# Kernel tuning notes

Hardware: AMD Instinct MI355X
Metric: run time of the kernel (lower is better)

## Reference

```python
import jax, jax.numpy as jnp
import numpy as np

IO, LAT, HID, NV = 64, 32, 60, 16

def setup_inputs() -> dict:
    key = jax.random.key(0)
    ks = jax.random.split(key, 11)
    def lin(k, fan_out, fan_in):
        kw, kb = jax.random.split(k)
        bound = 1.0 / np.sqrt(fan_in)
        w = jax.random.uniform(kw, (fan_out, fan_in), jnp.float32, -bound, bound)
        b = jax.random.uniform(kb, (fan_out,), jnp.float32, -bound, bound)
        return w, b
    enc1_w, enc1_b = lin(ks[0], HID, IO)
    mean_w, mean_b = lin(ks[1], LAT, HID)
    std_w, std_b = lin(ks[2], LAT, HID)
    dec1_w, dec1_b = lin(ks[3], HID, LAT)
    dec2_w, dec2_b = lin(ks[4], IO, HID)
    h_input = jax.random.normal(ks[5], (4096, 16, IO), jnp.float32)
    return {"h_input": h_input, "num_traj": 8,
            "enc1_w": enc1_w, "enc1_b": enc1_b, "mean_w": mean_w, "mean_b": mean_b,
            "std_w": std_w, "std_b": std_b, "dec1_w": dec1_w, "dec1_b": dec1_b,
            "dec2_w": dec2_w, "dec2_b": dec2_b}

def reference(h_input, num_traj, enc1_w, enc1_b, mean_w, mean_b, std_w, std_b, dec1_w, dec1_b, dec2_w, dec2_b):
    B, H, _ = h_input.shape
    x = h_input.reshape(-1, IO)               # [N, io]
    N = x.shape[0]
    h1 = jax.nn.relu(x @ enc1_w.T + enc1_b)   # [N, 60]
    mu = h1 @ mean_w.T + mean_b               # [N, L]
    logvar = h1 @ std_w.T + std_b             # [N, L]
    std = jnp.exp(0.5 * logvar)
    eps = jax.random.normal(jax.random.key(1), (num_traj, N, LAT), jnp.float32)
    z = mu[None] + eps * std[None]            # [T, N, L]
    # on-device closed-form standard-normal pdf (replaces scipy host roundtrip)
    log_pdf = -0.5 * (LAT * jnp.log(2.0 * jnp.pi) + jnp.sum(eps * eps, axis=-1))  # [T, N]
    pdf = jnp.exp(log_pdf)
    # decode, batched over trajectories
    h3 = jax.nn.relu(jnp.einsum('tnl,hl->tnh', z, dec1_w) + dec1_b)
    out = jnp.einsum('tnh,oh->tno', h3, dec2_w) + dec2_b          # [T, N, io]
    traj = out.reshape(num_traj, N, H, IO // H).transpose(0, 2, 1, 3)  # [T, H, N, io/H]
    p = jnp.exp(pdf)                          # faithful: exp of the pdf values
    p = p / jnp.sum(p, axis=0)                # normalize over trajectories
    prob_list = p.reshape(num_traj, -1, NV)   # [T, N/NV, NV]
    return traj, mu, logvar, prob_list
```

## Files before the change

kernel.cpp:

```cpp
#include <hip/hip_runtime.h>
#include <cstdint>


#define TPB_A 256
#define NBLK_A 1024
#define TPB_B 256
#define NBLK_B 2048

__device__ __forceinline__ void threefry2x32_01(uint32_t c0, uint32_t c1,
                                                uint32_t& o0, uint32_t& o1) {
  uint32_t x0 = c0;
  uint32_t x1 = c1 + 1u;
#define TFR(r) { x0 += x1; x1 = (x1 << (r)) | (x1 >> (32 - (r))); x1 ^= x0; }
  TFR(13) TFR(15) TFR(26) TFR(6)
  x0 += 1u;          x1 += 0x1BD11BDCu;
  TFR(17) TFR(29) TFR(16) TFR(24)
  x0 += 0x1BD11BDBu; x1 += 2u;
  TFR(13) TFR(15) TFR(26) TFR(6)
        x1 += 4u;
  TFR(17) TFR(29) TFR(16) TFR(24)
  x0 += 1u;          x1 += 0x1BD11BDFu;
  TFR(13) TFR(15) TFR(26) TFR(6)
  x0 += 0x1BD11BDBu; x1 += 5u;
#undef TFR
  o0 = x0; o1 = x1;
}

__device__ __forceinline__ uint32_t threefry_bits_partitionable(uint32_t idx) {
  uint32_t o0, o1;
  threefry2x32_01(0u, idx, o0, o1);
  return o0 ^ o1;
}

__device__ __forceinline__ float bits_to_normal(uint32_t b) {
  const float lo = -0.99999994f;
  float f = __uint_as_float((b >> 9) | 0x3F800000u) - 1.0f;
  float u = fmaxf(f * 2.0f + lo, lo);
  return 1.41421356f * erfinvf(u);
}

__global__ __launch_bounds__(TPB_A, 4) void vae_encode(
    const float* __restrict__ X,
    const float* __restrict__ w1, const float* __restrict__ b1,
    const float* __restrict__ wm, const float* __restrict__ bm,
    const float* __restrict__ wsd, const float* __restrict__ bsd,
    float* __restrict__ out) {
  const int tid = threadIdx.x;
  const int lane = tid & 63;
  const int slot = __builtin_amdgcn_readfirstlane(tid >> 6);
  const int i0 = slot * 8;
  const int n = blockIdx.x * 64 + lane;

  float x[64];
  {
    const float4* xr = (const float4*)(X + (size_t)n * 64);
#pragma unroll
    for (int q = 0; q < 16; ++q) {
      float4 v = xr[q];
      x[4 * q + 0] = v.x; x[4 * q + 1] = v.y;
      x[4 * q + 2] = v.z; x[4 * q + 3] = v.w;
    }
  }

  float mu[8], lv[8];
#pragma unroll
  for (int ii = 0; ii < 8; ++ii) { mu[ii] = bm[i0 + ii]; lv[ii] = bsd[i0 + ii]; }
  for (int j = 0; j < 60; ++j) {
    const float4* wr = (const float4*)(w1 + j * 64);
    float a0 = 0.f, a1 = 0.f, a2 = 0.f, a3 = 0.f;
#pragma unroll
    for (int q = 0; q < 16; ++q) {
      float4 w = wr[q];
      a0 = fmaf(w.x, x[4 * q + 0], a0);
      a1 = fmaf(w.y, x[4 * q + 1], a1);
      a2 = fmaf(w.z, x[4 * q + 2], a2);
      a3 = fmaf(w.w, x[4 * q + 3], a3);
    }
    float h = fmaxf((a0 + a1) + (a2 + a3) + b1[j], 0.f);
    const float* wmc = wm + i0 * 60 + j;
    const float* wsc = wsd + i0 * 60 + j;
#pragma unroll
    for (int ii = 0; ii < 8; ++ii) {
      mu[ii] = fmaf(wmc[ii * 60], h, mu[ii]);
      lv[ii] = fmaf(wsc[ii * 60], h, lv[ii]);
    }
  }

  float4* muo = (float4*)(out + (size_t)33554432 + (size_t)n * 32 + i0);
  float4* lvo = (float4*)(out + (size_t)35651584 + (size_t)n * 32 + i0);
  float4 v0, v1, w0, w1v;
  v0.x = mu[0]; v0.y = mu[1]; v0.z = mu[2]; v0.w = mu[3];
  v1.x = mu[4]; v1.y = mu[5]; v1.z = mu[6]; v1.w = mu[7];
  w0.x = lv[0]; w0.y = lv[1]; w0.z = lv[2]; w0.w = lv[3];
  w1v.x = lv[4]; w1v.y = lv[5]; w1v.z = lv[6]; w1v.w = lv[7];
  muo[0] = v0; muo[1] = v1;
  lvo[0] = w0; lvo[1] = w1v;
}

__global__ __launch_bounds__(TPB_B, 4) void vae_decode(
    const float* __restrict__ wd1, const float* __restrict__ bd1,
    const float* __restrict__ wd2, const float* __restrict__ bd2,
    float* __restrict__ out) {
  const int tid = threadIdx.x;
  const int g = blockIdx.x * TPB_B + tid;
  const int n = g & 65535;
  const int t = g >> 16;

  const float4* mur = (const float4*)(out + (size_t)33554432 + (size_t)n * 32);
  const float4* lvr = (const float4*)(out + (size_t)35651584 + (size_t)n * 32);
  const uint32_t cbase = (uint32_t)t * 2097152u + (uint32_t)n * 32u;
  float z[32];
#pragma unroll
  for (int gq = 0; gq < 8; ++gq) {
    float4 m4 = mur[gq];
    float4 v4 = lvr[gq];
    float s0 = expf(0.5f * v4.x), s1 = expf(0.5f * v4.y);
    float s2 = expf(0.5f * v4.z), s3 = expf(0.5f * v4.w);
    uint32_t c = cbase + (uint32_t)(4 * gq);
    z[4 * gq + 0] = fmaf(bits_to_normal(threefry_bits_partitionable(c + 0u)), s0, m4.x);
    z[4 * gq + 1] = fmaf(bits_to_normal(threefry_bits_partitionable(c + 1u)), s1, m4.y);
    z[4 * gq + 2] = fmaf(bits_to_normal(threefry_bits_partitionable(c + 2u)), s2, m4.z);
    z[4 * gq + 3] = fmaf(bits_to_normal(threefry_bits_partitionable(c + 3u)), s3, m4.w);
  }

  float h3[60];
#pragma unroll
  for (int j = 0; j < 60; ++j) {
    const float* wj = wd1 + j * 32;
    float a = bd1[j];
#pragma unroll
    for (int l = 0; l < 32; ++l) a = fmaf(wj[l], z[l], a);
    h3[j] = fmaxf(a, 0.f);
  }

  {
    float4* trj = (float4*)out + (size_t)(t * 16) * 65536 + n;
    const float4* bd24 = (const float4*)bd2;
    for (int hh = 0; hh < 16; ++hh) {
      const float4* w0 = (const float4*)(wd2 + (hh * 4 + 0) * 60);
      const float4* w1r = (const float4*)(wd2 + (hh * 4 + 1) * 60);
      const float4* w2 = (const float4*)(wd2 + (hh * 4 + 2) * 60);
      const float4* w3 = (const float4*)(wd2 + (hh * 4 + 3) * 60);
      float a0 = 0.f, a1 = 0.f, a2 = 0.f, a3 = 0.f;
#pragma unroll
      for (int q = 0; q < 15; ++q) {
        float4 wa = w0[q], wb = w1r[q], wc = w2[q], wdv = w3[q];
        float h0 = h3[4 * q + 0], hv1 = h3[4 * q + 1];
        float hv2 = h3[4 * q + 2], hv3 = h3[4 * q + 3];
        a0 = fmaf(wa.x, h0, a0); a0 = fmaf(wa.y, hv1, a0);
        a0 = fmaf(wa.z, hv2, a0); a0 = fmaf(wa.w, hv3, a0);
        a1 = fmaf(wb.x, h0, a1); a1 = fmaf(wb.y, hv1, a1);
        a1 = fmaf(wb.z, hv2, a1); a1 = fmaf(wb.w, hv3, a1);
        a2 = fmaf(wc.x, h0, a2); a2 = fmaf(wc.y, hv1, a2);
        a2 = fmaf(wc.z, hv2, a2); a2 = fmaf(wc.w, hv3, a2);
        a3 = fmaf(wdv.x, h0, a3); a3 = fmaf(wdv.y, hv1, a3);
        a3 = fmaf(wdv.z, hv2, a3); a3 = fmaf(wdv.w, hv3, a3);
      }
      float4 bb = bd24[hh];
      float4 o;
      o.x = a0 + bb.x; o.y = a1 + bb.y; o.z = a2 + bb.z; o.w = a3 + bb.w;
      trj[(size_t)hh * 65536] = o;
    }
  }

  out[(size_t)37748736 + (size_t)t * 65536 + (size_t)n] = 0.125f;
}

extern "C" void kernel_launch(void* const* d_in, const int* in_sizes, int n_in,
                              void* d_out, int out_size, void* d_ws, size_t ws_size,
                              hipStream_t stream) {
  const float* X   = (const float*)d_in[0];
  const float* w1  = (const float*)d_in[2];
  const float* b1  = (const float*)d_in[3];
  const float* wm  = (const float*)d_in[4];
  const float* bm  = (const float*)d_in[5];
  const float* wsd = (const float*)d_in[6];
  const float* bsd = (const float*)d_in[7];
  const float* wd1 = (const float*)d_in[8];
  const float* bd1 = (const float*)d_in[9];
  const float* wd2 = (const float*)d_in[10];
  const float* bd2 = (const float*)d_in[11];

  vae_encode<<<NBLK_A, TPB_A, 0, stream>>>(X, w1, b1, wm, bm, wsd, bsd,
                                           (float*)d_out);
  vae_decode<<<NBLK_B, TPB_B, 0, stream>>>(wd1, bd1, wd2, bd2, (float*)d_out);
}
```

Measured before the change: 388.0 us.

## Stage encoder weights in LDS with transposed mean/std layout; limit decoder unrolling

The encoder kernel now copies the first-layer weights and a transposed, interleaved copy of the mean/logvar weights into shared memory. This replaces per-thread global and scalar loads with vectorized LDS reads, cutting the number of weight loads in the inner loop. In the decoder, the hidden-layer loop changes from full unroll to unroll 2 and the output loop gets unroll 2, which may lower register pressure and code size. The costs are a block-level sync and staging work in the encoder, plus possibly less instruction-level parallelism in the decoder.

```diff
diff --git a/kernel.cpp b/kernel.cpp
--- a/kernel.cpp
+++ b/kernel.cpp
@@ -45,12 +45,26 @@
     const float* __restrict__ wm, const float* __restrict__ bm,
     const float* __restrict__ wsd, const float* __restrict__ bsd,
     float* __restrict__ out) {
+  __shared__ alignas(16) float s_w1[3840];
+  __shared__ alignas(16) float s_wmst[3840];
+
   const int tid = threadIdx.x;
   const int lane = tid & 63;
   const int slot = __builtin_amdgcn_readfirstlane(tid >> 6);
   const int i0 = slot * 8;
   const int n = blockIdx.x * 64 + lane;
 
+  {
+    const float4* w14 = (const float4*)w1;
+    float4* s14 = (float4*)s_w1;
+    for (int m = tid; m < 960; m += TPB_A) s14[m] = w14[m];
+    for (int m = tid; m < 3840; m += TPB_A) {
+      int j = m >> 6, i = m & 63;
+      s_wmst[m] = (i < 32) ? wm[i * 60 + j] : wsd[(i - 32) * 60 + j];
+    }
+  }
+  __syncthreads();
+
   float x[64];
   {
     const float4* xr = (const float4*)(X + (size_t)n * 64);
@@ -66,7 +80,7 @@
 #pragma unroll
   for (int ii = 0; ii < 8; ++ii) { mu[ii] = bm[i0 + ii]; lv[ii] = bsd[i0 + ii]; }
   for (int j = 0; j < 60; ++j) {
-    const float4* wr = (const float4*)(w1 + j * 64);
+    const float4* wr = (const float4*)&s_w1[j * 64];
     float a0 = 0.f, a1 = 0.f, a2 = 0.f, a3 = 0.f;
 #pragma unroll
     for (int q = 0; q < 16; ++q) {
@@ -77,13 +91,17 @@
       a3 = fmaf(w.w, x[4 * q + 3], a3);
     }
     float h = fmaxf((a0 + a1) + (a2 + a3) + b1[j], 0.f);
-    const float* wmc = wm + i0 * 60 + j;
-    const float* wsc = wsd + i0 * 60 + j;
-#pragma unroll
-    for (int ii = 0; ii < 8; ++ii) {
-      mu[ii] = fmaf(wmc[ii * 60], h, mu[ii]);
-      lv[ii] = fmaf(wsc[ii * 60], h, lv[ii]);
-    }
+    const float4* wa = (const float4*)&s_wmst[j * 64 + i0];
+    const float4* wc = (const float4*)&s_wmst[j * 64 + 32 + i0];
+    float4 A0 = wa[0], A1 = wa[1], C0 = wc[0], C1 = wc[1];
+    mu[0] = fmaf(A0.x, h, mu[0]); mu[1] = fmaf(A0.y, h, mu[1]);
+    mu[2] = fmaf(A0.z, h, mu[2]); mu[3] = fmaf(A0.w, h, mu[3]);
+    mu[4] = fmaf(A1.x, h, mu[4]); mu[5] = fmaf(A1.y, h, mu[5]);
+    mu[6] = fmaf(A1.z, h, mu[6]); mu[7] = fmaf(A1.w, h, mu[7]);
+    lv[0] = fmaf(C0.x, h, lv[0]); lv[1] = fmaf(C0.y, h, lv[1]);
+    lv[2] = fmaf(C0.z, h, lv[2]); lv[3] = fmaf(C0.w, h, lv[3]);
+    lv[4] = fmaf(C1.x, h, lv[4]); lv[5] = fmaf(C1.y, h, lv[5]);
+    lv[6] = fmaf(C1.z, h, lv[6]); lv[7] = fmaf(C1.w, h, lv[7]);
   }
 
   float4* muo = (float4*)(out + (size_t)33554432 + (size_t)n * 32 + i0);
@@ -124,7 +142,7 @@
   }
 
   float h3[60];
-#pragma unroll
+#pragma unroll 2
   for (int j = 0; j < 60; ++j) {
     const float* wj = wd1 + j * 32;
     float a = bd1[j];
@@ -136,6 +154,7 @@
   {
     float4* trj = (float4*)out + (size_t)(t * 16) * 65536 + n;
     const float4* bd24 = (const float4*)bd2;
+#pragma unroll 2
     for (int hh = 0; hh < 16; ++hh) {
       const float4* w0 = (const float4*)(wd2 + (hh * 4 + 0) * 60);
       const float4* w1r = (const float4*)(wd2 + (hh * 4 + 1) * 60);
```

New measurement: 726.3 us. 1.87x slower.
